# Kernel optimization log

Measured on AMD Instinct MI355X. Metric: run time of the kernel, lower is better.

The kernel has to match this reference:

```python
import jax, jax.numpy as jnp
import numpy as np

B = 1_000_000   # collocation points
N = 64          # layers[1]: number of tiny identity-init linear+activation layers
D = 3           # layers[0]: per-layer feature dim (rho, p, u columns)


def setup_inputs() -> dict:
    key = jax.random.key(0)
    k_x, k_w, k_cr, k_cp, k_cu = jax.random.split(key, 5)
    x = jax.random.normal(k_x, (B, D), dtype=jnp.float32)
    # Per-layer weights: identity init (as in the module) plus small noise so
    # the N layers are not all identical in the test harness.
    eye = jnp.eye(D, dtype=jnp.float32)
    W = eye[None, :, :] + 0.01 * jax.random.normal(k_w, (N, D, D), dtype=jnp.float32)
    b = jnp.zeros((N, D), dtype=jnp.float32)
    # Frozen output heads (Linear(N, 1, bias=False)), all initialized from c_initial.
    c_rho = jax.random.normal(k_cr, (1, N), dtype=jnp.float32)
    c_p = jax.random.normal(k_cp, (1, N), dtype=jnp.float32)
    c_u = jax.random.normal(k_cu, (1, N), dtype=jnp.float32)
    return {"x": x, "W": W, "b": b, "c_rho": c_rho, "c_p": c_p, "c_u": c_u}


def reference(x, W, b, c_rho, c_p, c_u):
    # Original loop: for i in range(N): u = act(Linear_i(x)); gather columns 0,1,2
    # and iteratively torch.cat them. Vectorized: one batched tiny GEMM over all
    # N layers, then slice the three channels.
    # x: [B, D]; W: [N, D, D]; b: [N, D] -> u: [B, N, D]
    u = jnp.tanh(jnp.einsum('bd,nkd->bnk', x, W) + b[None, :, :])
    u_rho = u[:, :, 0]   # [B, N]
    u_p = u[:, :, 1]
    u_u = u[:, :, 2]
    out_rho = u_rho @ c_rho.T   # [B, 1]
    out_p = u_p @ c_p.T
    out_u = u_u @ c_u.T
    return (out_rho, out_p, out_u)
```

## Files before the change

### kernel.cpp

```cpp
#include <hip/hip_runtime.h>


#define NN   64
#define RPT  2
#define BLK  256

typedef float f2 __attribute__((ext_vector_type(2)));

__device__ __forceinline__ f2 mk2(float a, float b) { f2 r; r.x = a; r.y = b; return r; }
__device__ __forceinline__ f2 pkfma(f2 a, f2 b, f2 c) { return __builtin_elementwise_fma(a, b, c); }

__device__ __forceinline__ float fexp2(float x) {
#if __has_builtin(__builtin_amdgcn_exp2f)
    return __builtin_amdgcn_exp2f(x);
#else
    return exp2f(x);
#endif
}
__device__ __forceinline__ float frcp(float x) {
#if __has_builtin(__builtin_amdgcn_rcpf)
    return __builtin_amdgcn_rcpf(x);
#else
    return 1.0f / x;
#endif
}

__global__ __launch_bounds__(BLK) void fused_tanh_heads(
    const float* __restrict__ x,
    const float* __restrict__ W,
    const float* __restrict__ bias,
    const float* __restrict__ c_rho,
    const float* __restrict__ c_p,
    const float* __restrict__ c_u,
    float* __restrict__ out,
    int B)
{
    __shared__ float sc[NN * 32];
    const int t = threadIdx.x;
    #pragma unroll
    for (int k = 0; k < 8; ++k) {
        const int idx = t + BLK * k;
        const int n = idx >> 5;
        const int o = idx & 31;
        const float K = 2.8853900817779268f;
        float v;
        if (o < 18)      v = W[n * 9 + (o >> 1)] * K;
        else if (o < 24) v = bias[n * 3 + ((o - 18) >> 1)] * K;
        else if (o < 26) v = c_rho[n];
        else if (o < 28) v = c_p[n];
        else if (o < 30) v = c_u[n];
        else             v = 0.0f;
        sc[idx] = v;
    }
    __syncthreads();

    float C0 = c_rho[t & 63], C1 = c_p[t & 63], C2 = c_u[t & 63];
    #pragma unroll
    for (int o = 1; o < 64; o <<= 1) {
        C0 += __shfl_xor(C0, o);
        C1 += __shfl_xor(C1, o);
        C2 += __shfl_xor(C2, o);
    }

    const int r0 = blockIdx.x * (BLK * RPT) + t;
    const int r1 = r0 + BLK;
    const bool ok0 = (r0 < B), ok1 = (r1 < B);

    const f2 X0 = mk2(ok0 ? x[r0 * 3 + 0] : 0.0f, ok1 ? x[r1 * 3 + 0] : 0.0f);
    const f2 X1 = mk2(ok0 ? x[r0 * 3 + 1] : 0.0f, ok1 ? x[r1 * 3 + 1] : 0.0f);
    const f2 X2 = mk2(ok0 ? x[r0 * 3 + 2] : 0.0f, ok1 ? x[r1 * 3 + 2] : 0.0f);

    f2 acc0 = mk2(0.0f, 0.0f), acc1 = acc0, acc2 = acc0;

    const float4* q4 = (const float4*)sc;
    #pragma unroll 2
    for (int n = 0; n < NN; ++n) {
        const float4 Q0 = q4[n * 8 + 0];
        const float4 Q1 = q4[n * 8 + 1];
        const float4 Q2 = q4[n * 8 + 2];
        const float4 Q3 = q4[n * 8 + 3];
        const float4 Q4 = q4[n * 8 + 4];
        const float4 Q5 = q4[n * 8 + 5];
        const float4 Q6 = q4[n * 8 + 6];
        const float4 Q7 = q4[n * 8 + 7];

        f2 h0 = pkfma(X2, mk2(Q1.x, Q1.y),
                 pkfma(X1, mk2(Q0.z, Q0.w),
                  pkfma(X0, mk2(Q0.x, Q0.y), mk2(Q4.z, Q4.w))));
        f2 h1 = pkfma(X2, mk2(Q2.z, Q2.w),
                 pkfma(X1, mk2(Q2.x, Q2.y),
                  pkfma(X0, mk2(Q1.z, Q1.w), mk2(Q5.x, Q5.y))));
        f2 h2 = pkfma(X2, mk2(Q4.x, Q4.y),
                 pkfma(X1, mk2(Q3.z, Q3.w),
                  pkfma(X0, mk2(Q3.x, Q3.y), mk2(Q5.z, Q5.w))));

        const float a00 = fexp2(h0.x) + 1.0f, a01 = fexp2(h0.y) + 1.0f;
        const float a10 = fexp2(h1.x) + 1.0f, a11 = fexp2(h1.y) + 1.0f;
        const float a20 = fexp2(h2.x) + 1.0f, a21 = fexp2(h2.y) + 1.0f;

        const float m0  = a00 * a10;
        const float rA  = frcp(m0 * a20);
        const float i20 = m0 * rA;
        const float s0  = a20 * rA;
        const float i00 = a10 * s0;
        const float i10 = a00 * s0;
        const float m1  = a01 * a11;
        const float rB  = frcp(m1 * a21);
        const float i21 = m1 * rB;
        const float s1  = a21 * rB;
        const float i01 = a11 * s1;
        const float i11 = a01 * s1;

        acc0 = pkfma(mk2(i00, i01), mk2(Q6.x, Q6.y), acc0);
        acc1 = pkfma(mk2(i10, i11), mk2(Q6.z, Q6.w), acc1);
        acc2 = pkfma(mk2(i20, i21), mk2(Q7.x, Q7.y), acc2);
    }

    if (ok0) {
        out[r0]         = fmaf(-2.0f, acc0.x, C0);
        out[B + r0]     = fmaf(-2.0f, acc1.x, C1);
        out[2 * B + r0] = fmaf(-2.0f, acc2.x, C2);
    }
    if (ok1) {
        out[r1]         = fmaf(-2.0f, acc0.y, C0);
        out[B + r1]     = fmaf(-2.0f, acc1.y, C1);
        out[2 * B + r1] = fmaf(-2.0f, acc2.y, C2);
    }
}

extern "C" void kernel_launch(void* const* d_in, const int* in_sizes, int n_in,
                              void* d_out, int out_size, void* d_ws, size_t ws_size,
                              hipStream_t stream) {
    (void)d_ws; (void)ws_size; (void)n_in; (void)out_size;
    const float* x     = (const float*)d_in[0];
    const float* W     = (const float*)d_in[1];
    const float* bias  = (const float*)d_in[2];
    const float* c_rho = (const float*)d_in[3];
    const float* c_p   = (const float*)d_in[4];
    const float* c_u   = (const float*)d_in[5];
    float* out = (float*)d_out;

    const int B = in_sizes[0] / 3;
    const int rows_per_block = BLK * RPT;
    const int grid = (B + rows_per_block - 1) / rows_per_block;

    fused_tanh_heads<<<grid, BLK, 0, stream>>>(x, W, bias, c_rho, c_p, c_u, out, B);
}
```

Measured before the change: 115.1 us.

## Precompute parameter table in setup kernel and read it via uniform global loads

```diff
diff --git a/kernel.cpp b/kernel.cpp
--- a/kernel.cpp
+++ b/kernel.cpp
@@ -25,42 +25,48 @@
 #endif
 }
 
-__global__ __launch_bounds__(BLK) void fused_tanh_heads(
-    const float* __restrict__ x,
-    const float* __restrict__ W,
-    const float* __restrict__ bias,
-    const float* __restrict__ c_rho,
-    const float* __restrict__ c_p,
-    const float* __restrict__ c_u,
-    float* __restrict__ out,
-    int B)
+__global__ __launch_bounds__(64) void setup_tab(
+    const float* __restrict__ W, const float* __restrict__ bias,
+    const float* __restrict__ c_rho, const float* __restrict__ c_p,
+    const float* __restrict__ c_u, float* __restrict__ ws)
 {
-    __shared__ float sc[NN * 32];
     const int t = threadIdx.x;
+    const float K = 2.8853900817779268f;
+    float* rec = ws + t * 32;
     #pragma unroll
-    for (int k = 0; k < 8; ++k) {
-        const int idx = t + BLK * k;
-        const int n = idx >> 5;
-        const int o = idx & 31;
-        const float K = 2.8853900817779268f;
-        float v;
-        if (o < 18)      v = W[n * 9 + (o >> 1)] * K;
-        else if (o < 24) v = bias[n * 3 + ((o - 18) >> 1)] * K;
-        else if (o < 26) v = c_rho[n];
-        else if (o < 28) v = c_p[n];
-        else if (o < 30) v = c_u[n];
-        else             v = 0.0f;
-        sc[idx] = v;
+    for (int j = 0; j < 9; ++j) {
+        const float w = W[t * 9 + j] * K;
+        rec[2 * j] = w; rec[2 * j + 1] = w;
     }
-    __syncthreads();
+    #pragma unroll
+    for (int k = 0; k < 3; ++k) {
+        const float b = bias[t * 3 + k] * K;
+        rec[18 + 2 * k] = b; rec[19 + 2 * k] = b;
+    }
+    const float cr = c_rho[t], cp = c_p[t], cu = c_u[t];
+    rec[24] = cr; rec[25] = cr;
+    rec[26] = cp; rec[27] = cp;
+    rec[28] = cu; rec[29] = cu;
+    rec[30] = 0.0f; rec[31] = 0.0f;
 
-    float C0 = c_rho[t & 63], C1 = c_p[t & 63], C2 = c_u[t & 63];
+    float C0 = cr, C1 = cp, C2 = cu;
     #pragma unroll
     for (int o = 1; o < 64; o <<= 1) {
         C0 += __shfl_xor(C0, o);
         C1 += __shfl_xor(C1, o);
         C2 += __shfl_xor(C2, o);
     }
+    if (t == 0) { ws[2048] = C0; ws[2049] = C1; ws[2050] = C2; }
+}
+
+__global__ __launch_bounds__(BLK) void fused_tanh_heads(
+    const float* __restrict__ x,
+    const float* __restrict__ ws,
+    float* __restrict__ out,
+    int B)
+{
+    const int t = threadIdx.x;
+    const float C0 = ws[2048], C1 = ws[2049], C2 = ws[2050];
 
     const int r0 = blockIdx.x * (BLK * RPT) + t;
     const int r1 = r0 + BLK;
@@ -71,49 +77,37 @@
     const f2 X2 = mk2(ok0 ? x[r0 * 3 + 2] : 0.0f, ok1 ? x[r1 * 3 + 2] : 0.0f);
 
     f2 acc0 = mk2(0.0f, 0.0f), acc1 = acc0, acc2 = acc0;
+    const f2 one2 = mk2(1.0f, 1.0f);
 
-    const float4* q4 = (const float4*)sc;
+    const f2* __restrict__ tab = (const f2*)ws;
     #pragma unroll 2
     for (int n = 0; n < NN; ++n) {
-        const float4 Q0 = q4[n * 8 + 0];
-        const float4 Q1 = q4[n * 8 + 1];
-        const float4 Q2 = q4[n * 8 + 2];
-        const float4 Q3 = q4[n * 8 + 3];
-        const float4 Q4 = q4[n * 8 + 4];
-        const float4 Q5 = q4[n * 8 + 5];
-        const float4 Q6 = q4[n * 8 + 6];
-        const float4 Q7 = q4[n * 8 + 7];
+        const f2* __restrict__ r = tab + n * 16;
+        const f2 w0 = r[0], w1 = r[1], w2 = r[2];
+        const f2 w3 = r[3], w4 = r[4], w5 = r[5];
+        const f2 w6 = r[6], w7 = r[7], w8 = r[8];
+        const f2 b0 = r[9], b1 = r[10], b2 = r[11];
+        const f2 cr = r[12], cp = r[13], cu = r[14];
 
-        f2 h0 = pkfma(X2, mk2(Q1.x, Q1.y),
-                 pkfma(X1, mk2(Q0.z, Q0.w),
-                  pkfma(X0, mk2(Q0.x, Q0.y), mk2(Q4.z, Q4.w))));
-        f2 h1 = pkfma(X2, mk2(Q2.z, Q2.w),
-                 pkfma(X1, mk2(Q2.x, Q2.y),
-                  pkfma(X0, mk2(Q1.z, Q1.w), mk2(Q5.x, Q5.y))));
-        f2 h2 = pkfma(X2, mk2(Q4.x, Q4.y),
-                 pkfma(X1, mk2(Q3.z, Q3.w),
-                  pkfma(X0, mk2(Q3.x, Q3.y), mk2(Q5.z, Q5.w))));
+        f2 h0 = pkfma(X2, w2, pkfma(X1, w1, pkfma(X0, w0, b0)));
+        f2 h1 = pkfma(X2, w5, pkfma(X1, w4, pkfma(X0, w3, b1)));
+        f2 h2 = pkfma(X2, w8, pkfma(X1, w7, pkfma(X0, w6, b2)));
 
-        const float a00 = fexp2(h0.x) + 1.0f, a01 = fexp2(h0.y) + 1.0f;
-        const float a10 = fexp2(h1.x) + 1.0f, a11 = fexp2(h1.y) + 1.0f;
-        const float a20 = fexp2(h2.x) + 1.0f, a21 = fexp2(h2.y) + 1.0f;
+        const f2 a0 = mk2(fexp2(h0.x), fexp2(h0.y)) + one2;
+        const f2 a1 = mk2(fexp2(h1.x), fexp2(h1.y)) + one2;
+        const f2 a2 = mk2(fexp2(h2.x), fexp2(h2.y)) + one2;
 
-        const float m0  = a00 * a10;
-        const float rA  = frcp(m0 * a20);
-        const float i20 = m0 * rA;
-        const float s0  = a20 * rA;
-        const float i00 = a10 * s0;
-        const float i10 = a00 * s0;
-        const float m1  = a01 * a11;
-        const float rB  = frcp(m1 * a21);
-        const float i21 = m1 * rB;
-        const float s1  = a21 * rB;
-        const float i01 = a11 * s1;
-        const float i11 = a01 * s1;
+        const f2 m = a0 * a1;
+        const f2 T = m * a2;
+        const f2 R = mk2(frcp(T.x), frcp(T.y));
+        const f2 i2 = m * R;
+        const f2 s  = a2 * R;
+        const f2 i0 = a1 * s;
+        const f2 i1 = a0 * s;
 
-        acc0 = pkfma(mk2(i00, i01), mk2(Q6.x, Q6.y), acc0);
-        acc1 = pkfma(mk2(i10, i11), mk2(Q6.z, Q6.w), acc1);
-        acc2 = pkfma(mk2(i20, i21), mk2(Q7.x, Q7.y), acc2);
+        acc0 = pkfma(i0, cr, acc0);
+        acc1 = pkfma(i1, cp, acc1);
+        acc2 = pkfma(i2, cu, acc2);
     }
 
     if (ok0) {
@@ -131,7 +125,7 @@
 extern "C" void kernel_launch(void* const* d_in, const int* in_sizes, int n_in,
                               void* d_out, int out_size, void* d_ws, size_t ws_size,
                               hipStream_t stream) {
-    (void)d_ws; (void)ws_size; (void)n_in; (void)out_size;
+    (void)ws_size; (void)n_in; (void)out_size;
     const float* x     = (const float*)d_in[0];
     const float* W     = (const float*)d_in[1];
     const float* bias  = (const float*)d_in[2];
@@ -139,10 +133,12 @@
     const float* c_p   = (const float*)d_in[4];
     const float* c_u   = (const float*)d_in[5];
     float* out = (float*)d_out;
+    float* ws  = (float*)d_ws;
 
     const int B = in_sizes[0] / 3;
     const int rows_per_block = BLK * RPT;
     const int grid = (B + rows_per_block - 1) / rows_per_block;
 
-    fused_tanh_heads<<<grid, BLK, 0, stream>>>(x, W, bias, c_rho, c_p, c_u, out, B);
+    setup_tab<<<1, 64, 0, stream>>>(W, bias, c_rho, c_p, c_u, ws);
+    fused_tanh_heads<<<grid, BLK, 0, stream>>>(x, ws, out, B);
 }
```

Measured after the change: 113.8 us. No clear change (-1.1%).
